# Kernel optimization log

Measured on AMD Instinct MI355X. Metric: run time of the kernel, lower is better.

## Reference

```python
import jax, jax.numpy as jnp
import numpy as np

B, S, H, NH, L, NS = 8, 4096, 768, 12, 2, 64
DH = H // NH
EPS = 1e-12


def _layer_norm(x, g, b):
    mu = jnp.mean(x, axis=-1, keepdims=True)
    var = jnp.mean((x - mu) ** 2, axis=-1, keepdims=True)
    return (x - mu) / jnp.sqrt(var + EPS) * g + b


def setup_inputs() -> dict:
    key = jax.random.key(0)
    ks = jax.random.split(key, 8)
    # sentence index per token: 64 equal contiguous sentences; position 0 is [CLS] in sentence 0
    sent_ind = jnp.broadcast_to((jnp.arange(S, dtype=jnp.int32) * NS) // S, (B, S)).astype(jnp.int32)
    start_layer = jax.random.normal(ks[0], (B, S, H), dtype=jnp.float32)
    init = lambda k, shape: (jax.random.normal(k, shape, dtype=jnp.float32) * 0.02)
    return {
        "sent_ind": sent_ind,
        "start_layer": start_layer,
        "Wq": init(ks[1], (L, H, H)), "bq": jnp.zeros((L, H), jnp.float32),
        "Wk": init(ks[2], (L, H, H)), "bk": jnp.zeros((L, H), jnp.float32),
        "Wv": init(ks[3], (L, H, H)), "bv": jnp.zeros((L, H), jnp.float32),
        "Wo": init(ks[4], (L, H, H)), "bo": jnp.zeros((L, H), jnp.float32),
        "ln_g": jnp.ones((L, H), jnp.float32), "ln_b": jnp.zeros((L, H), jnp.float32),
    }


def reference(sent_ind, start_layer, Wq, bq, Wk, bk, Wv, bv, Wo, bo, ln_g, ln_b):
    # ---- segment-mean pooling by sentence index (vectorized replacement of the python loops) ----
    onehot = (sent_ind[..., None] == jnp.arange(NS, dtype=sent_ind.dtype)).astype(start_layer.dtype)  # [B,S,NS]
    # the first [CLS] token is excluded from sentence 0's mean
    onehot = onehot.at[:, 0, :].set(0.0)
    sums = jnp.einsum('bsn,bsd->bnd', onehot, start_layer)          # [B,NS,H]
    counts = jnp.sum(onehot, axis=1)                                 # [B,NS]
    x = sums / counts[..., None]                                     # graph_vectors [B,NS,H]

    # ---- GAT layers: BertSelfAttention + GATSelfOutput(dense->gelu->LayerNorm), dropout=eval ----
    scale = 1.0 / (DH ** 0.5)
    for i in range(L):
        q = (x @ Wq[i] + bq[i]).reshape(B, NS, NH, DH)
        k = (x @ Wk[i] + bk[i]).reshape(B, NS, NH, DH)
        v = (x @ Wv[i] + bv[i]).reshape(B, NS, NH, DH)
        scores = jnp.einsum('bqhd,bkhd->bhqk', q, k) * scale
        probs = jax.nn.softmax(scores, axis=-1)
        ctx = jnp.einsum('bhqk,bkhd->bqhd', probs, v).reshape(B, NS, H)
        h = jax.nn.gelu(ctx @ Wo[i] + bo[i], approximate=False)
        x = _layer_norm(h, ln_g[i], ln_b[i])
    return x
```

## Files before the change

kernel.cpp:

```cpp
#include <hip/hip_runtime.h>
#include <hip/hip_bf16.h>

constexpr int cB  = 8;
constexpr int cS  = 4096;
constexpr int cH  = 768;
constexpr int cNH = 12;
constexpr int cL  = 2;
constexpr int cNS = 64;
constexpr int cDH = 64;
constexpr int cM  = cB * cNS;

typedef __attribute__((ext_vector_type(8))) short bf16x8;
typedef __attribute__((ext_vector_type(4))) float f32x4;
typedef __attribute__((ext_vector_type(4))) unsigned short u16x4;

__device__ __forceinline__ float b2f(unsigned short u) {
    union { float f; unsigned int i; } x; x.i = (unsigned int)u << 16; return x.f;
}
__device__ __forceinline__ unsigned short f2b(float f) {
    __hip_bfloat16 h = __float2bfloat16(f);
    return *(unsigned short*)&h;
}

union PrepShared {
    struct { int cnt; int list[cS]; float ps[192][4]; } p;
    float T[2][64][65];
};

__global__ __launch_bounds__(512) void prep_kernel(
    const int* __restrict__ sent_ind, const float* __restrict__ sl,
    __hip_bfloat16* __restrict__ xb,
    const float* __restrict__ Wq, const float* __restrict__ Wk,
    const float* __restrict__ Wv, const float* __restrict__ Wo,
    __hip_bfloat16* __restrict__ wt)
{
    __shared__ PrepShared sh;
    int tid = threadIdx.x;

    if (blockIdx.x < (unsigned)cM) {
        int bn = blockIdx.x;
        int b = bn >> 6, n = bn & (cNS - 1);
        if (tid == 0) sh.p.cnt = 0;
        __syncthreads();
        const int* si = sent_ind + (size_t)b * cS;
        for (int s = tid; s < cS; s += 512)
            if (s != 0 && si[s] == n) { int p = atomicAdd(&sh.p.cnt, 1); sh.p.list[p] = s; }
        __syncthreads();
        int c = sh.p.cnt;
        int grp = tid >> 8;
        int t   = tid & 255;
        int c0 = c >> 1;
        int lo = grp ? c0 : 0;
        int hi = grp ? c  : c0;
        float s0 = 0.f, s1 = 0.f, s2 = 0.f, s3 = 0.f;
        if (t < 192) {
            const float* bbase = sl + (size_t)b * cS * cH;
            int col = t * 4;
            float4 a0 = {0.f, 0.f, 0.f, 0.f};
            float4 a1 = {0.f, 0.f, 0.f, 0.f};
            float4 a2 = {0.f, 0.f, 0.f, 0.f};
            float4 a3 = {0.f, 0.f, 0.f, 0.f};
            int i = lo;
            for (; i + 4 <= hi; i += 4) {
                float4 r0 = *(const float4*)(bbase + (size_t)sh.p.list[i + 0] * cH + col);
                float4 r1 = *(const float4*)(bbase + (size_t)sh.p.list[i + 1] * cH + col);
                float4 r2 = *(const float4*)(bbase + (size_t)sh.p.list[i + 2] * cH + col);
                float4 r3 = *(const float4*)(bbase + (size_t)sh.p.list[i + 3] * cH + col);
                a0.x += r0.x; a0.y += r0.y; a0.z += r0.z; a0.w += r0.w;
                a1.x += r1.x; a1.y += r1.y; a1.z += r1.z; a1.w += r1.w;
                a2.x += r2.x; a2.y += r2.y; a2.z += r2.z; a2.w += r2.w;
                a3.x += r3.x; a3.y += r3.y; a3.z += r3.z; a3.w += r3.w;
            }
            for (; i < hi; ++i) {
                float4 r0 = *(const float4*)(bbase + (size_t)sh.p.list[i] * cH + col);
                a0.x += r0.x; a0.y += r0.y; a0.z += r0.z; a0.w += r0.w;
            }
            s0 = a0.x + a1.x + a2.x + a3.x;
            s1 = a0.y + a1.y + a2.y + a3.y;
            s2 = a0.z + a1.z + a2.z + a3.z;
            s3 = a0.w + a1.w + a2.w + a3.w;
        }
        if (grp == 1 && t < 192) {
            sh.p.ps[t][0] = s0; sh.p.ps[t][1] = s1;
            sh.p.ps[t][2] = s2; sh.p.ps[t][3] = s3;
        }
        __syncthreads();
        if (grp == 0 && t < 192) {
            float inv = 1.0f / (float)c;
            __hip_bfloat16* xr = xb + (size_t)bn * cH + t * 4;
            xr[0] = __float2bfloat16((s0 + sh.p.ps[t][0]) * inv);
            xr[1] = __float2bfloat16((s1 + sh.p.ps[t][1]) * inv);
            xr[2] = __float2bfloat16((s2 + sh.p.ps[t][2]) * inv);
            xr[3] = __float2bfloat16((s3 + sh.p.ps[t][3]) * inv);
        }
    } else {
        int sub = tid >> 8;
        int t   = tid & 255;
        int bi = (blockIdx.x - cM) * 2 + sub;
        int bx = bi % 12, by = (bi / 12) % 12, mat = bi / 144;
        int layer = mat >> 2, which = mat & 3;
        const float* W = (which == 0 ? Wq : which == 1 ? Wk : which == 2 ? Wv : Wo)
                         + (size_t)layer * cH * cH;
        int k0 = by * 64, n0 = bx * 64;
        int r = t >> 2, cb = (t & 3) * 16;
        #pragma unroll
        for (int u = 0; u < 4; ++u) {
            float4 w4 = *(const float4*)(W + (size_t)(k0 + r) * cH + n0 + cb + u * 4);
            sh.T[sub][r][cb + u * 4 + 0] = w4.x; sh.T[sub][r][cb + u * 4 + 1] = w4.y;
            sh.T[sub][r][cb + u * 4 + 2] = w4.z; sh.T[sub][r][cb + u * 4 + 3] = w4.w;
        }
        __syncthreads();
        int nn = t >> 2, kseg = (t & 3) * 16;
        __hip_bfloat16 tmp[16] __attribute__((aligned(16)));
        #pragma unroll
        for (int j = 0; j < 16; ++j)
            tmp[j] = __float2bfloat16(sh.T[sub][kseg + j][nn]);
        __hip_bfloat16* dst = wt + ((size_t)mat * cH + n0 + nn) * cH + k0 + kseg;
        *(bf16x8*)(dst)     = *(const bf16x8*)(tmp);
        *(bf16x8*)(dst + 8) = *(const bf16x8*)(tmp + 8);
    }
}

struct AttnShared {
    float QP[cNS][cDH + 4];
    float Ks[cNS][cDH + 4];
    float Vt[cDH][cNS + 4];
};

__global__ __launch_bounds__(256, 1) void qkvattn_kernel(
    const __hip_bfloat16* __restrict__ x_bf,
    const __hip_bfloat16* __restrict__ wqkv,
    const float* __restrict__ bq, const float* __restrict__ bk,
    const float* __restrict__ bv,
    __hip_bfloat16* __restrict__ ctx_bf)
{
    __shared__ AttnShared sh;
    int tid = threadIdx.x;
    int lane = tid & 63, wave = tid >> 6;
    int l15 = lane & 15, q4 = lane >> 4;
    int b = blockIdx.x / cNH, hh = blockIdx.x % cNH;

    const __hip_bfloat16* Arow[4];
    #pragma unroll
    for (int m = 0; m < 4; ++m)
        Arow[m] = x_bf + (size_t)(b * 64 + m * 16 + l15) * cH + q4 * 8;
    const __hip_bfloat16* Brow[3];
    int cmat[3], cnt_[3];
    #pragma unroll
    for (int j = 0; j < 3; ++j) {
        int c = wave * 3 + j;
        cmat[j] = c >> 2; cnt_[j] = c & 3;
        Brow[j] = wqkv + (size_t)cmat[j] * cH * cH
                       + (size_t)(hh * 64 + cnt_[j] * 16 + l15) * cH + q4 * 8;
    }

    f32x4 acc[3][4];
    #pragma unroll
    for (int j = 0; j < 3; ++j)
        #pragma unroll
        for (int m = 0; m < 4; ++m) acc[j][m] = (f32x4){0.f, 0.f, 0.f, 0.f};

    bf16x8 a[4], bb8[3], an[4], bn8[3];
    #pragma unroll
    for (int m = 0; m < 4; ++m) a[m] = *(const bf16x8*)(Arow[m]);
    #pragma unroll
    for (int j = 0; j < 3; ++j) bb8[j] = *(const bf16x8*)(Brow[j]);
    #pragma unroll
    for (int k0 = 0; k0 < cH; k0 += 32) {
        if (k0 + 32 < cH) {
            #pragma unroll
            for (int m = 0; m < 4; ++m) an[m] = *(const bf16x8*)(Arow[m] + k0 + 32);
            #pragma unroll
            for (int j = 0; j < 3; ++j) bn8[j] = *(const bf16x8*)(Brow[j] + k0 + 32);
        }
        #pragma unroll
        for (int j = 0; j < 3; ++j)
            #pragma unroll
            for (int m = 0; m < 4; ++m)
                acc[j][m] = __builtin_amdgcn_mfma_f32_16x16x32_bf16(a[m], bb8[j], acc[j][m], 0, 0, 0);
        #pragma unroll
        for (int m = 0; m < 4; ++m) a[m] = an[m];
        #pragma unroll
        for (int j = 0; j < 3; ++j) bb8[j] = bn8[j];
    }

    const float scale = 0.125f;
    #pragma unroll
    for (int j = 0; j < 3; ++j) {
        int mat = cmat[j], nt = cnt_[j];
        int col_d = nt * 16 + l15;
        int col_g = hh * 64 + col_d;
        float bias = (mat == 0 ? bq : mat == 1 ? bk : bv)[col_g];
        #pragma unroll
        for (int m = 0; m < 4; ++m) {
            #pragma unroll
            for (int r = 0; r < 4; ++r) {
                int row_s = m * 16 + q4 * 4 + r;
                float v = acc[j][m][r] + bias;
                if (mat == 0)      sh.QP[row_s][col_d] = v * scale;
                else if (mat == 1) sh.Ks[row_s][col_d] = v;
                else               sh.Vt[col_d][row_s] = v;
            }
        }
    }
    __syncthreads();

    int tx = tid & 15, ty = tid >> 4;
    float accs[4][4] = {};
    for (int d = 0; d < cDH; d += 4) {
        float4 qv[4], kv[4];
        #pragma unroll
        for (int i = 0; i < 4; ++i) qv[i] = *(const float4*)&sh.QP[ty * 4 + i][d];
        #pragma unroll
        for (int j = 0; j < 4; ++j) kv[j] = *(const float4*)&sh.Ks[tx + j * 16][d];
        #pragma unroll
        for (int i = 0; i < 4; ++i)
            #pragma unroll
            for (int j = 0; j < 4; ++j)
                accs[i][j] += qv[i].x * kv[j].x + qv[i].y * kv[j].y +
                              qv[i].z * kv[j].z + qv[i].w * kv[j].w;
    }
    __syncthreads();
    #pragma unroll
    for (int i = 0; i < 4; ++i)
        #pragma unroll
        for (int j = 0; j < 4; ++j)
            sh.QP[ty * 4 + i][tx + j * 16] = accs[i][j];
    __syncthreads();

    {
        int row = tid >> 2, jq = tid & 3;
        float e[16];
        float m = -1e30f;
        #pragma unroll
        for (int c = 0; c < 16; ++c) { e[c] = sh.QP[row][jq * 16 + c]; m = fmaxf(m, e[c]); }
        m = fmaxf(m, __shfl_xor(m, 1));
        m = fmaxf(m, __shfl_xor(m, 2));
        float s = 0.f;
        #pragma unroll
        for (int c = 0; c < 16; ++c) { e[c] = __expf(e[c] - m); s += e[c]; }
        s += __shfl_xor(s, 1);
        s += __shfl_xor(s, 2);
        float inv = 1.0f / s;
        #pragma unroll
        for (int c = 0; c < 16; ++c) sh.QP[row][jq * 16 + c] = e[c] * inv;
    }
    __syncthreads();

    float acco[4][4] = {};
    for (int c = 0; c < cNS; c += 4) {
        float4 p4[4], vt4[4];
        #pragma unroll
        for (int i = 0; i < 4; ++i) p4[i] = *(const float4*)&sh.QP[ty * 4 + i][c];
        #pragma unroll
        for (int j = 0; j < 4; ++j) vt4[j] = *(const float4*)&sh.Vt[tx + j * 16][c];
        #pragma unroll
        for (int i = 0; i < 4; ++i)
            #pragma unroll
            for (int j = 0; j < 4; ++j)
                acco[i][j] += p4[i].x * vt4[j].x + p4[i].y * vt4[j].y +
                              p4[i].z * vt4[j].z + p4[i].w * vt4[j].w;
    }
    size_t base = ((size_t)b * cNS) * cH + hh * cDH;
    #pragma unroll
    for (int i = 0; i < 4; ++i)
        #pragma unroll
        for (int j = 0; j < 4; ++j)
            ctx_bf[base + (size_t)(ty * 4 + i) * cH + tx + j * 16] =
                __float2bfloat16(acco[i][j]);
}

__global__ __launch_bounds__(512, 1) void ogemm_ln_kernel(
    const __hip_bfloat16* __restrict__ A,
    const __hip_bfloat16* __restrict__ Wt,
    const float* __restrict__ bias,
    const float* __restrict__ g, const float* __restrict__ bb,
    __hip_bfloat16* __restrict__ xb,
    float* __restrict__ outf)
{
    __shared__ unsigned short hs[16][776];
    int tid  = threadIdx.x;
    int lane = tid & 63;
    int wave = tid >> 6;
    int l15 = lane & 15, q4 = lane >> 4;
    int r0 = blockIdx.x * 16;
    int nb = wave * 96;

    const __hip_bfloat16* Arow = A  + (size_t)(r0 + l15) * cH + q4 * 8;
    const __hip_bfloat16* Wr   = Wt + (size_t)(nb + l15) * cH + q4 * 8;

    f32x4 acc[6];
    #pragma unroll
    for (int j = 0; j < 6; ++j) acc[j] = (f32x4){0.f, 0.f, 0.f, 0.f};

    bf16x8 a, bw[6], an, bn[6];
    a = *(const bf16x8*)(Arow);
    #pragma unroll
    for (int j = 0; j < 6; ++j) bw[j] = *(const bf16x8*)(Wr + (size_t)j * 16 * cH);
    #pragma unroll
    for (int k0 = 0; k0 < cH; k0 += 32) {
        if (k0 + 32 < cH) {
            an = *(const bf16x8*)(Arow + k0 + 32);
            #pragma unroll
            for (int j = 0; j < 6; ++j)
                bn[j] = *(const bf16x8*)(Wr + (size_t)j * 16 * cH + k0 + 32);
        }
        #pragma unroll
        for (int j = 0; j < 6; ++j)
            acc[j] = __builtin_amdgcn_mfma_f32_16x16x32_bf16(a, bw[j], acc[j], 0, 0, 0);
        a = an;
        #pragma unroll
        for (int j = 0; j < 6; ++j) bw[j] = bn[j];
    }

    #pragma unroll
    for (int j = 0; j < 6; ++j) {
        int col = nb + j * 16 + l15;
        float bv = bias[col];
        #pragma unroll
        for (int r = 0; r < 4; ++r) {
            float v = acc[j][r] + bv;
            v = 0.5f * v * (1.0f + erff(v * 0.70710678118654752f));
            hs[q4 * 4 + r][col] = f2b(v);
        }
    }
    __syncthreads();

    float gv[12], bv2[12];
    {
        const float* gp = g  + lane * 12;
        const float* bp = bb + lane * 12;
        #pragma unroll
        for (int j = 0; j < 3; ++j) {
            float4 g4 = *(const float4*)(gp + j * 4);
            float4 b4 = *(const float4*)(bp + j * 4);
            gv[j * 4 + 0] = g4.x; gv[j * 4 + 1] = g4.y;
            gv[j * 4 + 2] = g4.z; gv[j * 4 + 3] = g4.w;
            bv2[j * 4 + 0] = b4.x; bv2[j * 4 + 1] = b4.y;
            bv2[j * 4 + 2] = b4.z; bv2[j * 4 + 3] = b4.w;
        }
    }
    #pragma unroll
    for (int rr = 0; rr < 2; ++rr) {
        int lrow = wave * 2 + rr;
        int grow = r0 + lrow;
        const unsigned short* hr = &hs[lrow][lane * 12];
        float v[12];
        #pragma unroll
        for (int j = 0; j < 3; ++j) {
            u16x4 q = *(const u16x4*)(hr + j * 4);
            v[j * 4 + 0] = b2f(q[0]); v[j * 4 + 1] = b2f(q[1]);
            v[j * 4 + 2] = b2f(q[2]); v[j * 4 + 3] = b2f(q[3]);
        }
        float s = 0.f;
        #pragma unroll
        for (int j = 0; j < 12; ++j) s += v[j];
        #pragma unroll
        for (int o = 32; o; o >>= 1) s += __shfl_xor(s, o);
        float mu = s * (1.0f / 768.0f);
        float ss = 0.f;
        #pragma unroll
        for (int j = 0; j < 12; ++j) { v[j] -= mu; ss += v[j] * v[j]; }
        #pragma unroll
        for (int o = 32; o; o >>= 1) ss += __shfl_xor(ss, o);
        float var = ss * (1.0f / 768.0f);
        float inv = rsqrtf(var + 1e-12f);
        float o12[12];
        #pragma unroll
        for (int j = 0; j < 12; ++j) o12[j] = v[j] * inv * gv[j] + bv2[j];

        unsigned short* xr = (unsigned short*)(xb + (size_t)grow * cH) + lane * 12;
        #pragma unroll
        for (int j = 0; j < 3; ++j) {
            u16x4 q;
            q[0] = f2b(o12[j * 4 + 0]); q[1] = f2b(o12[j * 4 + 1]);
            q[2] = f2b(o12[j * 4 + 2]); q[3] = f2b(o12[j * 4 + 3]);
            *(u16x4*)(xr + j * 4) = q;
        }
        if (outf) {
            float* orow = outf + (size_t)grow * cH + lane * 12;
            #pragma unroll
            for (int j = 0; j < 3; ++j) {
                float4 o4 = { o12[j * 4 + 0], o12[j * 4 + 1],
                              o12[j * 4 + 2], o12[j * 4 + 3] };
                *(float4*)(orow + j * 4) = o4;
            }
        }
    }
}

extern "C" void kernel_launch(void* const* d_in, const int* in_sizes, int n_in,
                              void* d_out, int out_size, void* d_ws, size_t ws_size,
                              hipStream_t stream) {
    const int*   sent_ind = (const int*)d_in[0];
    const float* start    = (const float*)d_in[1];
    const float* Wq = (const float*)d_in[2];
    const float* bq = (const float*)d_in[3];
    const float* Wk = (const float*)d_in[4];
    const float* bk = (const float*)d_in[5];
    const float* Wv = (const float*)d_in[6];
    const float* bv = (const float*)d_in[7];
    const float* Wo = (const float*)d_in[8];
    const float* bo = (const float*)d_in[9];
    const float* ln_g = (const float*)d_in[10];
    const float* ln_b = (const float*)d_in[11];
    float* out = (float*)d_out;

    char* w = (char*)d_ws;
    __hip_bfloat16* wt     = (__hip_bfloat16*)w;
    __hip_bfloat16* x_bf   = (__hip_bfloat16*)(w + 9437184);
    __hip_bfloat16* ctx_bf = (__hip_bfloat16*)(w + 9437184 + 786432);

    prep_kernel<<<cM + 576, 512, 0, stream>>>(sent_ind, start, x_bf,
                                              Wq, Wk, Wv, Wo, wt);

    for (int i = 0; i < cL; ++i) {
        const __hip_bfloat16* wqkv = wt + (size_t)(i * 4) * cH * cH;
        const __hip_bfloat16* wto  = wt + (size_t)(i * 4 + 3) * cH * cH;
        qkvattn_kernel<<<cB * cNH, 256, 0, stream>>>(
            x_bf, wqkv, bq + (size_t)i * cH, bk + (size_t)i * cH, bv + (size_t)i * cH,
            ctx_bf);
        ogemm_ln_kernel<<<32, 512, 0, stream>>>(
            ctx_bf, wto, bo + (size_t)i * cH,
            ln_g + (size_t)i * cH, ln_b + (size_t)i * cH,
            x_bf, (i == cL - 1) ? out : nullptr);
    }
}
```

Before: 336.1 us.

## Use MFMA for attention and widen prep and QKV blocks

The prep kernel now runs 768 threads per block, splitting each sentence's token rows across four groups instead of two. Weight-transpose work is packed three tiles per block, which reduces that grid portion to 384 blocks. The QKV+attention kernel now uses 1024 threads, giving each wave one 16-row tile. It stores Q, K, V and the softmax probabilities as bf16 in shared memory and computes QK^T and PV with bf16 MFMA instead of scalar FP32 loops. This adds parallelism to the mostly serial per-block work, at the cost of extra bf16 rounding in the scores and probabilities.

```diff
diff --git a/kernel.cpp b/kernel.cpp
--- a/kernel.cpp
+++ b/kernel.cpp
@@ -23,11 +23,11 @@
 }
 
 union PrepShared {
-    struct { int cnt; int list[cS]; float ps[192][4]; } p;
-    float T[2][64][65];
+    struct { int cnt; int list[cS]; float ps[3][192][4]; } p;
+    float T[3][64][65];
 };
 
-__global__ __launch_bounds__(512) void prep_kernel(
+__global__ __launch_bounds__(768) void prep_kernel(
     const int* __restrict__ sent_ind, const float* __restrict__ sl,
     __hip_bfloat16* __restrict__ xb,
     const float* __restrict__ Wq, const float* __restrict__ Wk,
@@ -43,60 +43,61 @@
         if (tid == 0) sh.p.cnt = 0;
         __syncthreads();
         const int* si = sent_ind + (size_t)b * cS;
-        for (int s = tid; s < cS; s += 512)
+        for (int s = tid; s < cS; s += 768)
             if (s != 0 && si[s] == n) { int p = atomicAdd(&sh.p.cnt, 1); sh.p.list[p] = s; }
         __syncthreads();
         int c = sh.p.cnt;
-        int grp = tid >> 8;
-        int t   = tid & 255;
-        int c0 = c >> 1;
-        int lo = grp ? c0 : 0;
-        int hi = grp ? c  : c0;
-        float s0 = 0.f, s1 = 0.f, s2 = 0.f, s3 = 0.f;
-        if (t < 192) {
-            const float* bbase = sl + (size_t)b * cS * cH;
-            int col = t * 4;
-            float4 a0 = {0.f, 0.f, 0.f, 0.f};
-            float4 a1 = {0.f, 0.f, 0.f, 0.f};
-            float4 a2 = {0.f, 0.f, 0.f, 0.f};
-            float4 a3 = {0.f, 0.f, 0.f, 0.f};
-            int i = lo;
-            for (; i + 4 <= hi; i += 4) {
-                float4 r0 = *(const float4*)(bbase + (size_t)sh.p.list[i + 0] * cH + col);
-                float4 r1 = *(const float4*)(bbase + (size_t)sh.p.list[i + 1] * cH + col);
-                float4 r2 = *(const float4*)(bbase + (size_t)sh.p.list[i + 2] * cH + col);
-                float4 r3 = *(const float4*)(bbase + (size_t)sh.p.list[i + 3] * cH + col);
-                a0.x += r0.x; a0.y += r0.y; a0.z += r0.z; a0.w += r0.w;
-                a1.x += r1.x; a1.y += r1.y; a1.z += r1.z; a1.w += r1.w;
-                a2.x += r2.x; a2.y += r2.y; a2.z += r2.z; a2.w += r2.w;
-                a3.x += r3.x; a3.y += r3.y; a3.z += r3.z; a3.w += r3.w;
-            }
-            for (; i < hi; ++i) {
-                float4 r0 = *(const float4*)(bbase + (size_t)sh.p.list[i] * cH + col);
-                a0.x += r0.x; a0.y += r0.y; a0.z += r0.z; a0.w += r0.w;
-            }
-            s0 = a0.x + a1.x + a2.x + a3.x;
-            s1 = a0.y + a1.y + a2.y + a3.y;
-            s2 = a0.z + a1.z + a2.z + a3.z;
-            s3 = a0.w + a1.w + a2.w + a3.w;
-        }
-        if (grp == 1 && t < 192) {
-            sh.p.ps[t][0] = s0; sh.p.ps[t][1] = s1;
-            sh.p.ps[t][2] = s2; sh.p.ps[t][3] = s3;
+        int grp = tid / 192;
+        int t   = tid % 192;
+        int qtr = c >> 2;
+        int lo = grp * qtr;
+        int hi = (grp == 3) ? c : lo + qtr;
+        const float* bbase = sl + (size_t)b * cS * cH;
+        int col = t * 4;
+        float4 a0 = {0.f, 0.f, 0.f, 0.f};
+        float4 a1 = {0.f, 0.f, 0.f, 0.f};
+        float4 a2 = {0.f, 0.f, 0.f, 0.f};
+        float4 a3 = {0.f, 0.f, 0.f, 0.f};
+        int i = lo;
+        for (; i + 4 <= hi; i += 4) {
+            float4 r0 = *(const float4*)(bbase + (size_t)sh.p.list[i + 0] * cH + col);
+            float4 r1 = *(const float4*)(bbase + (size_t)sh.p.list[i + 1] * cH + col);
+            float4 r2 = *(const float4*)(bbase + (size_t)sh.p.list[i + 2] * cH + col);
+            float4 r3 = *(const float4*)(bbase + (size_t)sh.p.list[i + 3] * cH + col);
+            a0.x += r0.x; a0.y += r0.y; a0.z += r0.z; a0.w += r0.w;
+            a1.x += r1.x; a1.y += r1.y; a1.z += r1.z; a1.w += r1.w;
+            a2.x += r2.x; a2.y += r2.y; a2.z += r2.z; a2.w += r2.w;
+            a3.x += r3.x; a3.y += r3.y; a3.z += r3.z; a3.w += r3.w;
+        }
+        for (; i < hi; ++i) {
+            float4 r0 = *(const float4*)(bbase + (size_t)sh.p.list[i] * cH + col);
+            a0.x += r0.x; a0.y += r0.y; a0.z += r0.z; a0.w += r0.w;
+        }
+        float s0 = a0.x + a1.x + a2.x + a3.x;
+        float s1 = a0.y + a1.y + a2.y + a3.y;
+        float s2 = a0.z + a1.z + a2.z + a3.z;
+        float s3 = a0.w + a1.w + a2.w + a3.w;
+        if (grp) {
+            sh.p.ps[grp - 1][t][0] = s0; sh.p.ps[grp - 1][t][1] = s1;
+            sh.p.ps[grp - 1][t][2] = s2; sh.p.ps[grp - 1][t][3] = s3;
         }
         __syncthreads();
-        if (grp == 0 && t < 192) {
+        if (grp == 0) {
             float inv = 1.0f / (float)c;
-            __hip_bfloat16* xr = xb + (size_t)bn * cH + t * 4;
-            xr[0] = __float2bfloat16((s0 + sh.p.ps[t][0]) * inv);
-            xr[1] = __float2bfloat16((s1 + sh.p.ps[t][1]) * inv);
-            xr[2] = __float2bfloat16((s2 + sh.p.ps[t][2]) * inv);
-            xr[3] = __float2bfloat16((s3 + sh.p.ps[t][3]) * inv);
+            s0 += sh.p.ps[0][t][0] + sh.p.ps[1][t][0] + sh.p.ps[2][t][0];
+            s1 += sh.p.ps[0][t][1] + sh.p.ps[1][t][1] + sh.p.ps[2][t][1];
+            s2 += sh.p.ps[0][t][2] + sh.p.ps[1][t][2] + sh.p.ps[2][t][2];
+            s3 += sh.p.ps[0][t][3] + sh.p.ps[1][t][3] + sh.p.ps[2][t][3];
+            __hip_bfloat16* xr = xb + (size_t)bn * cH + col;
+            xr[0] = __float2bfloat16(s0 * inv);
+            xr[1] = __float2bfloat16(s1 * inv);
+            xr[2] = __float2bfloat16(s2 * inv);
+            xr[3] = __float2bfloat16(s3 * inv);
         }
     } else {
         int sub = tid >> 8;
         int t   = tid & 255;
-        int bi = (blockIdx.x - cM) * 2 + sub;
+        int bi = (blockIdx.x - cM) * 3 + sub;
         int bx = bi % 12, by = (bi / 12) % 12, mat = bi / 144;
         int layer = mat >> 2, which = mat & 3;
         const float* W = (which == 0 ? Wq : which == 1 ? Wk : which == 2 ? Wv : Wo)
@@ -121,153 +122,134 @@
     }
 }
 
-struct AttnShared {
-    float QP[cNS][cDH + 4];
-    float Ks[cNS][cDH + 4];
-    float Vt[cDH][cNS + 4];
+struct QAShared {
+    unsigned short Qs[cNS][72];
+    unsigned short Ks[cNS][72];
+    unsigned short Vt[cDH][72];
+    unsigned short P [cNS][72];
+    float S[cNS][68];
 };
 
-__global__ __launch_bounds__(256, 1) void qkvattn_kernel(
+__global__ __launch_bounds__(1024) void qkvattn2_kernel(
     const __hip_bfloat16* __restrict__ x_bf,
     const __hip_bfloat16* __restrict__ wqkv,
     const float* __restrict__ bq, const float* __restrict__ bk,
     const float* __restrict__ bv,
     __hip_bfloat16* __restrict__ ctx_bf)
 {
-    __shared__ AttnShared sh;
+    __shared__ QAShared sh;
     int tid = threadIdx.x;
     int lane = tid & 63, wave = tid >> 6;
     int l15 = lane & 15, q4 = lane >> 4;
-    int b = blockIdx.x / cNH, hh = blockIdx.x % cNH;
-
-    const __hip_bfloat16* Arow[4];
-    #pragma unroll
-    for (int m = 0; m < 4; ++m)
-        Arow[m] = x_bf + (size_t)(b * 64 + m * 16 + l15) * cH + q4 * 8;
+    int b = blockIdx.x / cNH, h = blockIdx.x % cNH;
+
+    int rowt = wave & 3;
+    int widx = wave >> 2;
+    int mats[3], colts[3];
     const __hip_bfloat16* Brow[3];
-    int cmat[3], cnt_[3];
     #pragma unroll
     for (int j = 0; j < 3; ++j) {
-        int c = wave * 3 + j;
-        cmat[j] = c >> 2; cnt_[j] = c & 3;
-        Brow[j] = wqkv + (size_t)cmat[j] * cH * cH
-                       + (size_t)(hh * 64 + cnt_[j] * 16 + l15) * cH + q4 * 8;
-    }
-
-    f32x4 acc[3][4];
-    #pragma unroll
-    for (int j = 0; j < 3; ++j)
-        #pragma unroll
-        for (int m = 0; m < 4; ++m) acc[j][m] = (f32x4){0.f, 0.f, 0.f, 0.f};
-
-    bf16x8 a[4], bb8[3], an[4], bn8[3];
-    #pragma unroll
-    for (int m = 0; m < 4; ++m) a[m] = *(const bf16x8*)(Arow[m]);
-    #pragma unroll
-    for (int j = 0; j < 3; ++j) bb8[j] = *(const bf16x8*)(Brow[j]);
-    #pragma unroll
+        int idx = widx * 3 + j;
+        mats[j] = idx >> 2; colts[j] = idx & 3;
+        Brow[j] = wqkv + (size_t)mats[j] * cH * cH
+                + (size_t)(h * 64 + colts[j] * 16 + l15) * cH + q4 * 8;
+    }
+    const __hip_bfloat16* Arow =
+        x_bf + (size_t)(b * 64 + rowt * 16 + l15) * cH + q4 * 8;
+
+    f32x4 acc[3];
+    #pragma unroll
+    for (int j = 0; j < 3; ++j) acc[j] = (f32x4){0.f, 0.f, 0.f, 0.f};
+
+    bf16x8 a, bw[3], an, bn[3];
+    a = *(const bf16x8*)(Arow);
+    #pragma unroll
+    for (int j = 0; j < 3; ++j) bw[j] = *(const bf16x8*)(Brow[j]);
+    #pragma unroll 4
     for (int k0 = 0; k0 < cH; k0 += 32) {
         if (k0 + 32 < cH) {
+            an = *(const bf16x8*)(Arow + k0 + 32);
             #pragma unroll
-            for (int m = 0; m < 4; ++m) an[m] = *(const bf16x8*)(Arow[m] + k0 + 32);
-            #pragma unroll
-            for (int j = 0; j < 3; ++j) bn8[j] = *(const bf16x8*)(Brow[j] + k0 + 32);
+            for (int j = 0; j < 3; ++j) bn[j] = *(const bf16x8*)(Brow[j] + k0 + 32);
         }
         #pragma unroll
         for (int j = 0; j < 3; ++j)
-            #pragma unroll
-            for (int m = 0; m < 4; ++m)
-                acc[j][m] = __builtin_amdgcn_mfma_f32_16x16x32_bf16(a[m], bb8[j], acc[j][m], 0, 0, 0);
-        #pragma unroll
-        for (int m = 0; m < 4; ++m) a[m] = an[m];
-        #pragma unroll
-        for (int j = 0; j < 3; ++j) bb8[j] = bn8[j];
-    }
-
-    const float scale = 0.125f;
+            acc[j] = __builtin_amdgcn_mfma_f32_16x16x32_bf16(a, bw[j], acc[j], 0, 0, 0);
+        a = an;
+        #pragma unroll
+        for (int j = 0; j < 3; ++j) bw[j] = bn[j];
+    }
+
     #pragma unroll
     for (int j = 0; j < 3; ++j) {
-        int mat = cmat[j], nt = cnt_[j];
-        int col_d = nt * 16 + l15;
-        int col_g = hh * 64 + col_d;
-        float bias = (mat == 0 ? bq : mat == 1 ? bk : bv)[col_g];
-        #pragma unroll
-        for (int m = 0; m < 4; ++m) {
-            #pragma unroll
-            for (int r = 0; r < 4; ++r) {
-                int row_s = m * 16 + q4 * 4 + r;
-                float v = acc[j][m][r] + bias;
-                if (mat == 0)      sh.QP[row_s][col_d] = v * scale;
-                else if (mat == 1) sh.Ks[row_s][col_d] = v;
-                else               sh.Vt[col_d][row_s] = v;
-            }
+        int mat = mats[j], colt = colts[j];
+        int col_d = colt * 16 + l15;
+        float bias = (mat == 0 ? bq : mat == 1 ? bk : bv)[h * 64 + col_d];
+        #pragma unroll
+        for (int r = 0; r < 4; ++r) {
+            int row_s = rowt * 16 + q4 * 4 + r;
+            float v = acc[j][r] + bias;
+            if (mat == 0)      sh.Qs[row_s][col_d] = f2b(v * 0.125f);
+            else if (mat == 1) sh.Ks[row_s][col_d] = f2b(v);
+            else               sh.Vt[col_d][row_s] = f2b(v);
         }
     }
     __syncthreads();
 
-    int tx = tid & 15, ty = tid >> 4;
-    float accs[4][4] = {};
-    for (int d = 0; d < cDH; d += 4) {
-        float4 qv[4], kv[4];
-        #pragma unroll
-        for (int i = 0; i < 4; ++i) qv[i] = *(const float4*)&sh.QP[ty * 4 + i][d];
-        #pragma unroll
-        for (int j = 0; j < 4; ++j) kv[j] = *(const float4*)&sh.Ks[tx + j * 16][d];
-        #pragma unroll
-        for (int i = 0; i < 4; ++i)
-            #pragma unroll
-            for (int j = 0; j < 4; ++j)
-                accs[i][j] += qv[i].x * kv[j].x + qv[i].y * kv[j].y +
-                              qv[i].z * kv[j].z + qv[i].w * kv[j].w;
+    {
+        int rt = wave >> 2, ct = wave & 3;
+        bf16x8 aq0 = *(const bf16x8*)&sh.Qs[rt * 16 + l15][q4 * 8];
+        bf16x8 aq1 = *(const bf16x8*)&sh.Qs[rt * 16 + l15][32 + q4 * 8];
+        bf16x8 bk0 = *(const bf16x8*)&sh.Ks[ct * 16 + l15][q4 * 8];
+        bf16x8 bk1 = *(const bf16x8*)&sh.Ks[ct * 16 + l15][32 + q4 * 8];
+        f32x4 sc = (f32x4){0.f, 0.f, 0.f, 0.f};
+        sc = __builtin_amdgcn_mfma_f32_16x16x32_bf16(aq0, bk0, sc, 0, 0, 0);
+        sc = __builtin_amdgcn_mfma_f32_16x16x32_bf16(aq1, bk1, sc, 0, 0, 0);
+        #pragma unroll
+        for (int r = 0; r < 4; ++r)
+            sh.S[rt * 16 + q4 * 4 + r][ct * 16 + l15] = sc[r];
     }
     __syncthreads();
-    #pragma unroll
-    for (int i = 0; i < 4; ++i)
-        #pragma unroll
-        for (int j = 0; j < 4; ++j)
-            sh.QP[ty * 4 + i][tx + j * 16] = accs[i][j];
-    __syncthreads();
 
     {
-        int row = tid >> 2, jq = tid & 3;
-        float e[16];
+        int row = tid >> 4, jq = tid & 15;
+        float e[4];
         float m = -1e30f;
         #pragma unroll
-        for (int c = 0; c < 16; ++c) { e[c] = sh.QP[row][jq * 16 + c]; m = fmaxf(m, e[c]); }
+        for (int c = 0; c < 4; ++c) { e[c] = sh.S[row][jq * 4 + c]; m = fmaxf(m, e[c]); }
         m = fmaxf(m, __shfl_xor(m, 1));
         m = fmaxf(m, __shfl_xor(m, 2));
+        m = fmaxf(m, __shfl_xor(m, 4));
+        m = fmaxf(m, __shfl_xor(m, 8));
         float s = 0.f;
         #pragma unroll
-        for (int c = 0; c < 16; ++c) { e[c] = __expf(e[c] - m); s += e[c]; }
+        for (int c = 0; c < 4; ++c) { e[c] = __expf(e[c] - m); s += e[c]; }
         s += __shfl_xor(s, 1);
         s += __shfl_xor(s, 2);
+        s += __shfl_xor(s, 4);
+        s += __shfl_xor(s, 8);
         float inv = 1.0f / s;
         #pragma unroll
-        for (int c = 0; c < 16; ++c) sh.QP[row][jq * 16 + c] = e[c] * inv;
+        for (int c = 0; c < 4; ++c) sh.P[row][jq * 4 + c] = f2b(e[c] * inv);
     }
     __syncthreads();
 
-    float acco[4][4] = {};
-    for (int c = 0; c < cNS; c += 4) {
-        float4 p4[4], vt4[4];
-        #pragma unroll
-        for (int i = 0; i < 4; ++i) p4[i] = *(const float4*)&sh.QP[ty * 4 + i][c];
-        #pragma unroll
-        for (int j = 0; j < 4; ++j) vt4[j] = *(const float4*)&sh.Vt[tx + j * 16][c];
-        #pragma unroll
-        for (int i = 0; i < 4; ++i)
-            #pragma unroll
-            for (int j = 0; j < 4; ++j)
-                acco[i][j] += p4[i].x * vt4[j].x + p4[i].y * vt4[j].y +
-                              p4[i].z * vt4[j].z + p4[i].w * vt4[j].w;
-    }
-    size_t base = ((size_t)b * cNS) * cH + hh * cDH;
-    #pragma unroll
-    for (int i = 0; i < 4; ++i)
-        #pragma unroll
-        for (int j = 0; j < 4; ++j)
-            ctx_bf[base + (size_t)(ty * 4 + i) * cH + tx + j * 16] =
-                __float2bfloat16(acco[i][j]);
+    {
+        int rt = wave >> 2, ct = wave & 3;
+        bf16x8 ap0 = *(const bf16x8*)&sh.P[rt * 16 + l15][q4 * 8];
+        bf16x8 ap1 = *(const bf16x8*)&sh.P[rt * 16 + l15][32 + q4 * 8];
+        bf16x8 bv0 = *(const bf16x8*)&sh.Vt[ct * 16 + l15][q4 * 8];
+        bf16x8 bv1 = *(const bf16x8*)&sh.Vt[ct * 16 + l15][32 + q4 * 8];
+        f32x4 o = (f32x4){0.f, 0.f, 0.f, 0.f};
+        o = __builtin_amdgcn_mfma_f32_16x16x32_bf16(ap0, bv0, o, 0, 0, 0);
+        o = __builtin_amdgcn_mfma_f32_16x16x32_bf16(ap1, bv1, o, 0, 0, 0);
+        #pragma unroll
+        for (int r = 0; r < 4; ++r) {
+            int q = rt * 16 + q4 * 4 + r;
+            ctx_bf[(size_t)(b * cNS + q) * cH + h * cDH + ct * 16 + l15] =
+                __float2bfloat16(o[r]);
+        }
+    }
 }
 
 __global__ __launch_bounds__(512, 1) void ogemm_ln_kernel(
@@ -407,17 +389,18 @@
     float* out = (float*)d_out;
 
     char* w = (char*)d_ws;
+    const size_t MH = 786432;
     __hip_bfloat16* wt     = (__hip_bfloat16*)w;
     __hip_bfloat16* x_bf   = (__hip_bfloat16*)(w + 9437184);
-    __hip_bfloat16* ctx_bf = (__hip_bfloat16*)(w + 9437184 + 786432);
-
-    prep_kernel<<<cM + 576, 512, 0, stream>>>(sent_ind, start, x_bf,
+    __hip_bfloat16* ctx_bf = (__hip_bfloat16*)(w + 9437184 + MH);
+
+    prep_kernel<<<cM + 384, 768, 0, stream>>>(sent_ind, start, x_bf,
                                               Wq, Wk, Wv, Wo, wt);
 
     for (int i = 0; i < cL; ++i) {
         const __hip_bfloat16* wqkv = wt + (size_t)(i * 4) * cH * cH;
         const __hip_bfloat16* wto  = wt + (size_t)(i * 4 + 3) * cH * cH;
-        qkvattn_kernel<<<cB * cNH, 256, 0, stream>>>(
+        qkvattn2_kernel<<<cB * cNH, 1024, 0, stream>>>(
             x_bf, wqkv, bq + (size_t)i * cH, bk + (size_t)i * cH, bv + (size_t)i * cH,
             ctx_bf);
         ogemm_ln_kernel<<<32, 512, 0, stream>>>(
```

Result: slower. 367.6 us (+9.4%).
